# Optimization experiments

Measured on AMD Instinct MI355X. Metric: run time of the kernel, lower is better.

The kernel has to match this reference:

```python
import jax, jax.numpy as jnp
import numpy as np

N_NODES = 50000
IN_C, HID_C, OUT_C = 128, 128, 64
N_EDGES = 800000
N_LABEL = 200000
BN_EPS = 1e-5


def setup_inputs() -> dict:
    key = jax.random.key(0)
    ks = jax.random.split(key, 12)
    s = lambda fan_in: 1.0 / np.sqrt(fan_in)
    return {
        "x": jax.random.normal(ks[0], (N_NODES, IN_C), dtype=jnp.float32),
        "edge_index": jax.random.randint(ks[1], (2, N_EDGES), 0, N_NODES, dtype=jnp.int64),
        "edge_label_index": jax.random.randint(ks[2], (2, N_LABEL), 0, N_NODES, dtype=jnp.int64),
        # SAGEConv1: lin_l (neighbor branch, with bias) and lin_r (root branch, no bias)
        "W1l": jax.random.uniform(ks[3], (IN_C, HID_C), jnp.float32, -s(IN_C), s(IN_C)),
        "W1r": jax.random.uniform(ks[4], (IN_C, HID_C), jnp.float32, -s(IN_C), s(IN_C)),
        "b1": jax.random.uniform(ks[5], (HID_C,), jnp.float32, -s(IN_C), s(IN_C)),
        # BatchNorm1d(hidden)
        "gamma": jnp.ones((HID_C,), jnp.float32),
        "beta": jnp.zeros((HID_C,), jnp.float32),
        # SAGEConv2
        "W2l": jax.random.uniform(ks[6], (HID_C, OUT_C), jnp.float32, -s(HID_C), s(HID_C)),
        "W2r": jax.random.uniform(ks[7], (HID_C, OUT_C), jnp.float32, -s(HID_C), s(HID_C)),
        "b2": jax.random.uniform(ks[8], (OUT_C,), jnp.float32, -s(HID_C), s(HID_C)),
    }


def _sage_conv(x, edge_index, Wl, Wr, b):
    # PyG SAGEConv(aggr='mean'): out = lin_l(mean_{j->i} x_j) + lin_r(x_i)
    src, dst = edge_index[0], edge_index[1]
    n = x.shape[0]
    agg = jax.ops.segment_sum(x[src], dst, num_segments=n)          # [N, C]
    cnt = jax.ops.segment_sum(jnp.ones((src.shape[0],), x.dtype), dst, num_segments=n)
    mean = agg / jnp.maximum(cnt, 1.0)[:, None]                     # isolated nodes -> 0
    return mean @ Wl + x @ Wr + b


def _batchnorm(h, gamma, beta):
    mu = jnp.mean(h, axis=0)
    var = jnp.mean((h - mu) ** 2, axis=0)  # biased variance (torch BN training math)
    return gamma * (h - mu) * jax.lax.rsqrt(var + BN_EPS) + beta


def reference(x, edge_index, edge_label_index, W1l, W1r, b1, gamma, beta, W2l, W2r, b2):
    h = _sage_conv(x, edge_index, W1l, W1r, b1)
    h = jax.nn.relu(_batchnorm(h, gamma, beta))
    # dropout is identity in inference mode
    z = _sage_conv(h, edge_index, W2l, W2r, b2)
    src = z[edge_label_index[0]]
    dst = z[edge_label_index[1]]
    return jnp.sum(src * dst, axis=-1)  # [E_label]
```

## Files before the change

kernel.cpp:

```cpp
#include <hip/hip_runtime.h>

constexpr int N_NODES = 50000;
constexpr int IN_C    = 128;
constexpr int HID_C   = 128;
constexpr int OUT_C   = 64;
constexpr int N_EDGES = 800000;
constexpr int N_LABEL = 200000;
constexpr float BN_EPS = 1e-5f;
constexpr int NCHUNK  = (N_NODES + 256) / 256 + 1;
constexpr int BN_BLOCKS = 512;
constexpr int BN_RPH    = 13;

typedef __attribute__((ext_vector_type(8))) short bf16x8;
typedef __attribute__((ext_vector_type(4))) float f32x4;

__device__ __forceinline__ float bf_lo(unsigned v) {
    union { unsigned u; float f; } t; t.u = v << 16; return t.f;
}
__device__ __forceinline__ float bf_hi(unsigned v) {
    union { unsigned u; float f; } t; t.u = v & 0xffff0000u; return t.f;
}
__device__ __forceinline__ unsigned short f2bf(float f) {
    union { float f; unsigned u; } t; t.f = f;
    unsigned r = t.u + 0x7fffu + ((t.u >> 16) & 1u);
    return (unsigned short)(r >> 16);
}
__device__ __forceinline__ unsigned pack2bf(float a, float b) {
    return (unsigned)f2bf(a) | ((unsigned)f2bf(b) << 16);
}

__device__ __forceinline__ float fp8_f32(unsigned b) {
    union { unsigned u; float f; } t;
    t.u = ((b & 0x80u) << 24) | ((b & 0x7Fu) << 20);
    return t.f * 0x1p120f;
}
__device__ __forceinline__ unsigned f32_fp8(float x) {
    union { float f; unsigned u; } t; t.f = x * 0x1p-120f;
    unsigned au = t.u & 0x7FFFFFFFu;
    unsigned r = au + 0x7FFFFu + ((au >> 20) & 1u);
    return ((r >> 20) & 0x7Fu) | ((t.u >> 24) & 0x80u);
}

__global__ void zero_kernel(int* __restrict__ ideg, float* __restrict__ sums) {
    int i = blockIdx.x * 256 + threadIdx.x;
    if (i < 50432) ideg[i] = 0;
    if (i < 256) sums[i] = 0.f;
}

__global__ void hist_kernel(const int* __restrict__ dst, int* __restrict__ deg,
                            int* __restrict__ rank) {
    int e = blockIdx.x * blockDim.x + threadIdx.x;
    if (e < N_EDGES) rank[e] = atomicAdd(&deg[dst[e]], 1);
}

__global__ void chunk_sum_kernel(const int* __restrict__ deg, int* __restrict__ bsum) {
    int i = blockIdx.x * 256 + threadIdx.x;
    int v = deg[i];
    #pragma unroll
    for (int o = 32; o > 0; o >>= 1) v += __shfl_down(v, o, 64);
    __shared__ int ws[4];
    if ((threadIdx.x & 63) == 0) ws[threadIdx.x >> 6] = v;
    __syncthreads();
    if (threadIdx.x == 0) bsum[blockIdx.x] = ws[0] + ws[1] + ws[2] + ws[3];
}

__global__ void scan_bsum_kernel(const int* __restrict__ bsum, int* __restrict__ boff) {
    __shared__ int t[256];
    int tid = threadIdx.x;
    t[tid] = (tid < NCHUNK) ? bsum[tid] : 0;
    __syncthreads();
    for (int o = 1; o < 256; o <<= 1) {
        int v = t[tid];
        int add = (tid >= o) ? t[tid - o] : 0;
        __syncthreads();
        t[tid] = v + add;
        __syncthreads();
    }
    boff[tid] = (tid == 0) ? 0 : t[tid - 1];
}

__global__ void scan_final_kernel(const int* __restrict__ deg, const int* __restrict__ boff,
                                  int* __restrict__ off) {
    __shared__ int t[256];
    int tid = threadIdx.x;
    int i = blockIdx.x * 256 + tid;
    int d = deg[i];
    t[tid] = d;
    __syncthreads();
    for (int o = 1; o < 256; o <<= 1) {
        int v = t[tid];
        int add = (tid >= o) ? t[tid - o] : 0;
        __syncthreads();
        t[tid] = v + add;
        __syncthreads();
    }
    int excl = boff[blockIdx.x] + t[tid] - d;
    if (i <= N_NODES) off[i] = excl;
}

__global__ void scatter_kernel(const int* __restrict__ src, const int* __restrict__ dst,
                               const int* __restrict__ off, const int* __restrict__ rank,
                               int* __restrict__ csr_src) {
    int e = blockIdx.x * blockDim.x + threadIdx.x;
    if (e < N_EDGES) csr_src[off[dst[e]] + rank[e]] = src[e];
}

__global__ void prep_B(const float* __restrict__ Wl, const float* __restrict__ Wr,
                       short* __restrict__ Bp, int C) {
    int f = blockIdx.x * 256 + threadIdx.x;
    if (f >= 128 * C) return;
    int HALF = C >> 1;
    int j = f & 7;
    int l = (f >> 3) & 63;
    int ktnt = f >> 9;
    int kt = ktnt & 3, nt = ktnt >> 2;
    int n = nt * 16 + (l & 15);
    int k = kt * 32 + ((l >> 4) << 3) + j;
    float v = (n < HALF) ? Wl[k * HALF + n] : Wr[k * HALF + (n - HALF)];
    Bp[f] = (short)f2bf(v);
}

template <int MODE>
__global__ __launch_bounds__(256) void mfma_gemm(
    const void* __restrict__ Ain, const short* __restrict__ Bp,
    const float* __restrict__ bias, const float* __restrict__ ss,
    unsigned char* __restrict__ outFp8,
    unsigned short* __restrict__ outL16,
    unsigned short* __restrict__ outH16)
{
    constexpr int C    = (MODE == 0) ? 256 : 128;
    constexpr int NT   = C / 16;
    constexpr int HALF = C / 2;
    constexpr int CHUNKS = 128 * C / 8;

    __shared__ short sB[128 * C];

    {
        const float4* bp4 = reinterpret_cast<const float4*>(Bp);
        float4* sb4 = reinterpret_cast<float4*>(sB);
        #pragma unroll
        for (int i = 0; i < CHUNKS / 256; ++i)
            sb4[i * 256 + threadIdx.x] = bp4[i * 256 + threadIdx.x];
    }

    int tid  = threadIdx.x;
    int wid  = tid >> 6, lane = tid & 63;
    int m0   = blockIdx.x * 64 + wid * 16;
    int row  = m0 + (lane & 15);
    int rowc = (row < N_NODES) ? row : (N_NODES - 1);
    int kbase = (lane >> 4) * 8;

    bf16x8 a[4];
    #pragma unroll
    for (int kt = 0; kt < 4; ++kt) {
        int k0 = kt * 32 + kbase;
        float v[8];
        if (MODE == 0) {
            const float* ap = (const float*)Ain + (long long)rowc * 128;
            float4 u0 = *reinterpret_cast<const float4*>(ap + k0);
            float4 u1 = *reinterpret_cast<const float4*>(ap + k0 + 4);
            v[0]=u0.x; v[1]=u0.y; v[2]=u0.z; v[3]=u0.w;
            v[4]=u1.x; v[5]=u1.y; v[6]=u1.z; v[7]=u1.w;
        } else {
            const unsigned short* ap = (const unsigned short*)Ain + (long long)rowc * 128;
            uint4 w = *reinterpret_cast<const uint4*>(ap + k0);
            v[0]=bf_lo(w.x); v[1]=bf_hi(w.x); v[2]=bf_lo(w.y); v[3]=bf_hi(w.y);
            v[4]=bf_lo(w.z); v[5]=bf_hi(w.z); v[6]=bf_lo(w.w); v[7]=bf_hi(w.w);
            float4 s0 = *reinterpret_cast<const float4*>(ss + k0);
            float4 s1 = *reinterpret_cast<const float4*>(ss + k0 + 4);
            float4 t0 = *reinterpret_cast<const float4*>(ss + 128 + k0);
            float4 t1 = *reinterpret_cast<const float4*>(ss + 128 + k0 + 4);
            float sc[8] = {s0.x, s0.y, s0.z, s0.w, s1.x, s1.y, s1.z, s1.w};
            float sh[8] = {t0.x, t0.y, t0.z, t0.w, t1.x, t1.y, t1.z, t1.w};
            #pragma unroll
            for (int j = 0; j < 8; ++j) v[j] = fmaxf(v[j] * sc[j] + sh[j], 0.f);
        }
        #pragma unroll
        for (int j = 0; j < 8; ++j) a[kt][j] = (short)f2bf(v[j]);
    }

    __syncthreads();

    f32x4 acc[NT] = {};
    #pragma unroll
    for (int kt = 0; kt < 4; ++kt) {
        #pragma unroll
        for (int nt = 0; nt < NT; ++nt) {
            bf16x8 b = *reinterpret_cast<const bf16x8*>(
                sB + ((((nt << 2) + kt) * 64 + lane) << 3));
            acc[nt] = __builtin_amdgcn_mfma_f32_16x16x32_bf16(a[kt], b, acc[nt], 0, 0, 0);
        }
    }

    int r0 = m0 + ((lane >> 4) << 2);
    int nl = lane & 15;
    #pragma unroll
    for (int nt = 0; nt < NT; ++nt) {
        int col = nt * 16 + nl;
        float bb = (col >= HALF) ? bias[col - HALF] : 0.f;
        #pragma unroll
        for (int j = 0; j < 4; ++j) {
            int r = r0 + j;
            if (r >= N_NODES) continue;
            float vv = acc[nt][j];
            if (MODE == 0) {
                if (col < HALF) outFp8[(long long)r * 128 + col] = (unsigned char)f32_fp8(vv);
                else            outH16[(long long)r * 128 + (col - HALF)] = f2bf(vv + bb);
            } else {
                if (col < HALF) outL16[(long long)r * 64 + col] = f2bf(vv);
                else            outH16[(long long)r * 64 + (col - HALF)] = f2bf(vv + bb);
            }
        }
    }
}

__global__ __launch_bounds__(256) void agg_mean_add_128(
    const int* __restrict__ off, const int* __restrict__ csr_src,
    const uint2* __restrict__ y8, uint4* __restrict__ h4) {
    int node = blockIdx.x * 4 + (threadIdx.x >> 6);
    if (node >= N_NODES) return;
    int lane = threadIdx.x & 63;
    int grp  = lane >> 4;
    int c8   = lane & 15;
    int beg = off[node], end = off[node + 1];
    float s[8] = {0.f, 0.f, 0.f, 0.f, 0.f, 0.f, 0.f, 0.f};
    int i = beg + grp;
    for (; i + 4 < end; i += 8) {
        uint2 v0 = y8[(long long)csr_src[i]     * 16 + c8];
        uint2 v1 = y8[(long long)csr_src[i + 4] * 16 + c8];
        #pragma unroll
        for (int j = 0; j < 4; ++j) {
            s[j]     += fp8_f32((v0.x >> (8 * j)) & 0xFFu) + fp8_f32((v1.x >> (8 * j)) & 0xFFu);
            s[4 + j] += fp8_f32((v0.y >> (8 * j)) & 0xFFu) + fp8_f32((v1.y >> (8 * j)) & 0xFFu);
        }
    }
    for (; i < end; i += 4) {
        uint2 v0 = y8[(long long)csr_src[i] * 16 + c8];
        #pragma unroll
        for (int j = 0; j < 4; ++j) {
            s[j]     += fp8_f32((v0.x >> (8 * j)) & 0xFFu);
            s[4 + j] += fp8_f32((v0.y >> (8 * j)) & 0xFFu);
        }
    }
    #pragma unroll
    for (int j = 0; j < 8; ++j) {
        s[j] += __shfl_down(s[j], 16);
        s[j] += __shfl_down(s[j], 32);
    }
    if (grp == 0) {
        float inv = (end > beg) ? 1.0f / (float)(end - beg) : 0.f;
        uint4 hv = h4[(long long)node * 16 + c8];
        hv.x = pack2bf(bf_lo(hv.x) + s[0] * inv, bf_hi(hv.x) + s[1] * inv);
        hv.y = pack2bf(bf_lo(hv.y) + s[2] * inv, bf_hi(hv.y) + s[3] * inv);
        hv.z = pack2bf(bf_lo(hv.z) + s[4] * inv, bf_hi(hv.z) + s[5] * inv);
        hv.w = pack2bf(bf_lo(hv.w) + s[6] * inv, bf_hi(hv.w) + s[7] * inv);
        h4[(long long)node * 16 + c8] = hv;
    }
}

__global__ __launch_bounds__(256) void bn_stats_partial(
    const uint2* __restrict__ h2, float* __restrict__ partial) {
    int tid = threadIdx.x;
    int wid = tid >> 6;
    int lane = tid & 63;
    int half = lane >> 5;
    int c4   = lane & 31;
    int hw   = (blockIdx.x << 3) + (wid << 1) + half;
    int r0   = hw * BN_RPH;

    uint2 v[BN_RPH];
    #pragma unroll
    for (int j = 0; j < BN_RPH; ++j) {
        int r = r0 + j;
        v[j] = (r < N_NODES) ? h2[(long long)r * 32 + c4] : uint2{0u, 0u};
    }
    float s[4] = {0.f, 0.f, 0.f, 0.f}, q[4] = {0.f, 0.f, 0.f, 0.f};
    #pragma unroll
    for (int j = 0; j < BN_RPH; ++j) {
        float a0 = bf_lo(v[j].x), a1 = bf_hi(v[j].x);
        float a2 = bf_lo(v[j].y), a3 = bf_hi(v[j].y);
        s[0] += a0; q[0] += a0 * a0;
        s[1] += a1; q[1] += a1 * a1;
        s[2] += a2; q[2] += a2 * a2;
        s[3] += a3; q[3] += a3 * a3;
    }
    #pragma unroll
    for (int j = 0; j < 4; ++j) {
        s[j] += __shfl_down(s[j], 32);
        q[j] += __shfl_down(q[j], 32);
    }
    __shared__ float ls[4][32][8];
    if (half == 0) {
        #pragma unroll
        for (int j = 0; j < 4; ++j) { ls[wid][c4][j] = s[j]; ls[wid][c4][4 + j] = q[j]; }
    }
    __syncthreads();
    if (tid < 32) {
        #pragma unroll
        for (int j = 0; j < 8; ++j) {
            float a = ls[0][tid][j] + ls[1][tid][j] + ls[2][tid][j] + ls[3][tid][j];
            partial[blockIdx.x * 256 + (j < 4 ? 0 : 128) + tid * 4 + (j & 3)] = a;
        }
    }
}

__global__ void bn_stats_reduce(const float* __restrict__ partial,
                                float* __restrict__ sums) {
    int t = threadIdx.x;
    int b0 = blockIdx.x * (BN_BLOCKS / 16);
    float a = 0.f;
    #pragma unroll 8
    for (int b = b0; b < b0 + BN_BLOCKS / 16; ++b)
        a += partial[b * 256 + t];
    atomicAdd(&sums[t], a);
}

__global__ void bn_finalize_kernel(const float* __restrict__ sums,
                                   const float* __restrict__ gamma,
                                   const float* __restrict__ beta,
                                   float* __restrict__ ss) {
    int c = threadIdx.x;
    float mu  = sums[c] * (1.0f / N_NODES);
    float var = sums[128 + c] * (1.0f / N_NODES) - mu * mu;
    float sc = gamma[c] * rsqrtf(var + BN_EPS);
    ss[c] = sc;
    ss[128 + c] = beta[c] - mu * sc;
}

__global__ __launch_bounds__(256) void agg_mean_add_64(
    const int* __restrict__ off, const int* __restrict__ csr_src,
    const uint2* __restrict__ t2l2, const uint2* __restrict__ t2r2,
    uint2* __restrict__ z2) {
    int node = blockIdx.x * 4 + (threadIdx.x >> 6);
    if (node >= N_NODES) return;
    int lane = threadIdx.x & 63;
    int grp  = lane >> 4;
    int c8   = lane & 15;
    int beg = off[node], end = off[node + 1];
    float s0 = 0.f, s1 = 0.f, s2 = 0.f, s3 = 0.f;
    int i = beg + grp;
    for (; i + 4 < end; i += 8) {
        uint2 v0 = t2l2[(long long)csr_src[i]     * 16 + c8];
        uint2 v1 = t2l2[(long long)csr_src[i + 4] * 16 + c8];
        s0 += bf_lo(v0.x) + bf_lo(v1.x);
        s1 += bf_hi(v0.x) + bf_hi(v1.x);
        s2 += bf_lo(v0.y) + bf_lo(v1.y);
        s3 += bf_hi(v0.y) + bf_hi(v1.y);
    }
    for (; i < end; i += 4) {
        uint2 v0 = t2l2[(long long)csr_src[i] * 16 + c8];
        s0 += bf_lo(v0.x); s1 += bf_hi(v0.x);
        s2 += bf_lo(v0.y); s3 += bf_hi(v0.y);
    }
    s0 += __shfl_down(s0, 16); s1 += __shfl_down(s1, 16);
    s2 += __shfl_down(s2, 16); s3 += __shfl_down(s3, 16);
    s0 += __shfl_down(s0, 32); s1 += __shfl_down(s1, 32);
    s2 += __shfl_down(s2, 32); s3 += __shfl_down(s3, 32);
    if (grp == 0) {
        float inv = (end > beg) ? 1.0f / (float)(end - beg) : 0.f;
        uint2 rv = t2r2[(long long)node * 16 + c8];
        uint2 o;
        o.x = pack2bf(bf_lo(rv.x) + s0 * inv, bf_hi(rv.x) + s1 * inv);
        o.y = pack2bf(bf_lo(rv.y) + s2 * inv, bf_hi(rv.y) + s3 * inv);
        z2[(long long)node * 16 + c8] = o;
    }
}

__global__ void edge_dot_kernel(const int* __restrict__ eli,
                                const unsigned short* __restrict__ z,
                                float* __restrict__ out) {
    long long gid = (long long)blockIdx.x * blockDim.x + threadIdx.x;
    int l = (int)(gid >> 4);
    int lane = (int)(gid & 15);
    if (l >= N_LABEL) return;
    int s = eli[l];
    int d = eli[N_LABEL + l];
    uint2 av = *reinterpret_cast<const uint2*>(z + (long long)s * 64 + lane * 4);
    uint2 bv = *reinterpret_cast<const uint2*>(z + (long long)d * 64 + lane * 4);
    float p = bf_lo(av.x) * bf_lo(bv.x) + bf_hi(av.x) * bf_hi(bv.x)
            + bf_lo(av.y) * bf_lo(bv.y) + bf_hi(av.y) * bf_hi(bv.y);
    p += __shfl_down(p, 8, 16);
    p += __shfl_down(p, 4, 16);
    p += __shfl_down(p, 2, 16);
    p += __shfl_down(p, 1, 16);
    if (lane == 0) out[l] = p;
}

extern "C" void kernel_launch(void* const* d_in, const int* in_sizes, int n_in,
                              void* d_out, int out_size, void* d_ws, size_t ws_size,
                              hipStream_t stream) {
    const float* x     = (const float*)d_in[0];
    const int*   ei    = (const int*)d_in[1];
    const int*   eli   = (const int*)d_in[2];
    const float* W1l   = (const float*)d_in[3];
    const float* W1r   = (const float*)d_in[4];
    const float* b1    = (const float*)d_in[5];
    const float* gamma = (const float*)d_in[6];
    const float* beta  = (const float*)d_in[7];
    const float* W2l   = (const float*)d_in[8];
    const float* W2r   = (const float*)d_in[9];
    const float* b2    = (const float*)d_in[10];
    float* out = (float*)d_out;

    const int* src  = ei;
    const int* dstv = ei + N_EDGES;

    int* ideg  = (int*)d_ws;
    int* ioff  = ideg + 50432;
    int* ibsum = ioff + 50056;
    int* iboff = ibsum + 256;
    int* icsr  = iboff + 256;
    unsigned char*  y1  = (unsigned char*)(icsr + 800000);
    unsigned short* h   = (unsigned short*)(y1 + 6400000);
    unsigned short* t2l = h + 6400000;
    unsigned short* t2r = t2l + 3200000;
    unsigned short* z   = t2r + 3200000;
    float* sums = (float*)(z + 3200000);
    float* ss   = sums + 256;
    short* Bp1  = (short*)(ss + 256);
    short* Bp2  = Bp1 + 32768;
    float* bnpart = (float*)(Bp2 + 16384);
    int* irank = (int*)y1;

    zero_kernel<<<(50432 + 255) / 256, 256, 0, stream>>>(ideg, sums);

    prep_B<<<(128 * 256 + 255) / 256, 256, 0, stream>>>(W1l, W1r, Bp1, 256);
    prep_B<<<(128 * 128 + 255) / 256, 256, 0, stream>>>(W2l, W2r, Bp2, 128);

    hist_kernel<<<(N_EDGES + 255) / 256, 256, 0, stream>>>(dstv, ideg, irank);
    chunk_sum_kernel<<<NCHUNK, 256, 0, stream>>>(ideg, ibsum);
    scan_bsum_kernel<<<1, 256, 0, stream>>>(ibsum, iboff);
    scan_final_kernel<<<NCHUNK, 256, 0, stream>>>(ideg, iboff, ioff);
    scatter_kernel<<<(N_EDGES + 255) / 256, 256, 0, stream>>>(src, dstv, ioff, irank, icsr);

    const int GEMM_GRID = (N_NODES + 63) / 64;

    mfma_gemm<0><<<GEMM_GRID, 256, 0, stream>>>(x, Bp1, b1, ss, y1, nullptr, h);
    agg_mean_add_128<<<(N_NODES + 3) / 4, 256, 0, stream>>>(
        ioff, icsr, (const uint2*)y1, (uint4*)h);

    bn_stats_partial<<<BN_BLOCKS, 256, 0, stream>>>((const uint2*)h, bnpart);
    bn_stats_reduce<<<16, 256, 0, stream>>>(bnpart, sums);
    bn_finalize_kernel<<<1, 128, 0, stream>>>(sums, gamma, beta, ss);

    mfma_gemm<1><<<GEMM_GRID, 256, 0, stream>>>(h, Bp2, b2, ss, nullptr, t2l, t2r);
    agg_mean_add_64<<<(N_NODES + 3) / 4, 256, 0, stream>>>(
        ioff, icsr, (const uint2*)t2l, (const uint2*)t2r, (uint2*)z);

    edge_dot_kernel<<<((long long)N_LABEL * 16 + 255) / 256, 256, 0, stream>>>(eli, z, out);
}
```

Measured before the change: 187.9 us.

## Fuse BatchNorm statistics into layer-1 aggregation and merge setup kernels

Accumulates per-channel sum and sum-of-squares inside the first mean-aggregation kernel, whose blocks now each process 32 nodes. This removes the separate bn_stats_partial pass that re-read the whole hidden matrix. The zeroing and both weight-packing kernels are merged into one launch, and the GEMM blocks grow to 512 threads covering 128 rows. In exchange, the partial-stats buffer grows to one slot per aggregation block, there are fewer aggregation blocks to spread across the GPU, and each block runs a serial loop over its nodes.

```diff
diff --git a/kernel.cpp b/kernel.cpp
--- a/kernel.cpp
+++ b/kernel.cpp
@@ -8,8 +8,7 @@
 constexpr int N_LABEL = 200000;
 constexpr float BN_EPS = 1e-5f;
 constexpr int NCHUNK  = (N_NODES + 256) / 256 + 1;
-constexpr int BN_BLOCKS = 512;
-constexpr int BN_RPH    = 13;
+constexpr int AGG_BLOCKS = (N_NODES + 31) / 32;
 
 typedef __attribute__((ext_vector_type(8))) short bf16x8;
 typedef __attribute__((ext_vector_type(4))) float f32x4;
@@ -41,10 +40,32 @@
     return ((r >> 20) & 0x7Fu) | ((t.u >> 24) & 0x80u);
 }
 
-__global__ void zero_kernel(int* __restrict__ ideg, float* __restrict__ sums) {
+__global__ void setup_kernel(int* __restrict__ ideg, float* __restrict__ sums,
+                             const float* __restrict__ W1l, const float* __restrict__ W1r,
+                             short* __restrict__ Bp1,
+                             const float* __restrict__ W2l, const float* __restrict__ W2r,
+                             short* __restrict__ Bp2) {
     int i = blockIdx.x * 256 + threadIdx.x;
     if (i < 50432) ideg[i] = 0;
     if (i < 256) sums[i] = 0.f;
+    int j = i & 7;
+    int l = (i >> 3) & 63;
+    int ktnt = i >> 9;
+    int kt = ktnt & 3;
+    int nl = l & 15, kk = ((l >> 4) << 3) + j;
+    int k = kt * 32 + kk;
+    if (i < 32768) {
+        int nt = ktnt >> 2;
+        int n = nt * 16 + nl;
+        float v = (n < 128) ? W1l[k * 128 + n] : W1r[k * 128 + (n - 128)];
+        Bp1[i] = (short)f2bf(v);
+    }
+    if (i < 16384) {
+        int nt = ktnt >> 2;
+        int n = nt * 16 + nl;
+        float v = (n < 64) ? W2l[k * 64 + n] : W2r[k * 64 + (n - 64)];
+        Bp2[i] = (short)f2bf(v);
+    }
 }
 
 __global__ void hist_kernel(const int* __restrict__ dst, int* __restrict__ deg,
@@ -105,23 +126,8 @@
     if (e < N_EDGES) csr_src[off[dst[e]] + rank[e]] = src[e];
 }
 
-__global__ void prep_B(const float* __restrict__ Wl, const float* __restrict__ Wr,
-                       short* __restrict__ Bp, int C) {
-    int f = blockIdx.x * 256 + threadIdx.x;
-    if (f >= 128 * C) return;
-    int HALF = C >> 1;
-    int j = f & 7;
-    int l = (f >> 3) & 63;
-    int ktnt = f >> 9;
-    int kt = ktnt & 3, nt = ktnt >> 2;
-    int n = nt * 16 + (l & 15);
-    int k = kt * 32 + ((l >> 4) << 3) + j;
-    float v = (n < HALF) ? Wl[k * HALF + n] : Wr[k * HALF + (n - HALF)];
-    Bp[f] = (short)f2bf(v);
-}
-
 template <int MODE>
-__global__ __launch_bounds__(256) void mfma_gemm(
+__global__ __launch_bounds__(512) void mfma_gemm(
     const void* __restrict__ Ain, const short* __restrict__ Bp,
     const float* __restrict__ bias, const float* __restrict__ ss,
     unsigned char* __restrict__ outFp8,
@@ -139,13 +145,13 @@
         const float4* bp4 = reinterpret_cast<const float4*>(Bp);
         float4* sb4 = reinterpret_cast<float4*>(sB);
         #pragma unroll
-        for (int i = 0; i < CHUNKS / 256; ++i)
-            sb4[i * 256 + threadIdx.x] = bp4[i * 256 + threadIdx.x];
+        for (int i = 0; i < CHUNKS / 512; ++i)
+            sb4[i * 512 + threadIdx.x] = bp4[i * 512 + threadIdx.x];
     }
 
     int tid  = threadIdx.x;
     int wid  = tid >> 6, lane = tid & 63;
-    int m0   = blockIdx.x * 64 + wid * 16;
+    int m0   = blockIdx.x * 128 + wid * 16;
     int row  = m0 + (lane & 15);
     int rowc = (row < N_NODES) ? row : (N_NODES - 1);
     int kbase = (lane >> 4) * 8;
@@ -214,103 +220,82 @@
     }
 }
 
-__global__ __launch_bounds__(256) void agg_mean_add_128(
+__global__ __launch_bounds__(256) void agg_mean_add_128_bn(
     const int* __restrict__ off, const int* __restrict__ csr_src,
-    const uint2* __restrict__ y8, uint4* __restrict__ h4) {
-    int node = blockIdx.x * 4 + (threadIdx.x >> 6);
-    if (node >= N_NODES) return;
-    int lane = threadIdx.x & 63;
+    const uint2* __restrict__ y8, uint4* __restrict__ h4,
+    float* __restrict__ partial) {
+    int tid  = threadIdx.x;
+    int wid  = tid >> 6;
+    int lane = tid & 63;
     int grp  = lane >> 4;
     int c8   = lane & 15;
-    int beg = off[node], end = off[node + 1];
-    float s[8] = {0.f, 0.f, 0.f, 0.f, 0.f, 0.f, 0.f, 0.f};
-    int i = beg + grp;
-    for (; i + 4 < end; i += 8) {
-        uint2 v0 = y8[(long long)csr_src[i]     * 16 + c8];
-        uint2 v1 = y8[(long long)csr_src[i + 4] * 16 + c8];
-        #pragma unroll
-        for (int j = 0; j < 4; ++j) {
-            s[j]     += fp8_f32((v0.x >> (8 * j)) & 0xFFu) + fp8_f32((v1.x >> (8 * j)) & 0xFFu);
-            s[4 + j] += fp8_f32((v0.y >> (8 * j)) & 0xFFu) + fp8_f32((v1.y >> (8 * j)) & 0xFFu);
-        }
-    }
-    for (; i < end; i += 4) {
-        uint2 v0 = y8[(long long)csr_src[i] * 16 + c8];
-        #pragma unroll
-        for (int j = 0; j < 4; ++j) {
-            s[j]     += fp8_f32((v0.x >> (8 * j)) & 0xFFu);
-            s[4 + j] += fp8_f32((v0.y >> (8 * j)) & 0xFFu);
-        }
-    }
-    #pragma unroll
-    for (int j = 0; j < 8; ++j) {
-        s[j] += __shfl_down(s[j], 16);
-        s[j] += __shfl_down(s[j], 32);
-    }
+    float rs[8] = {0.f,0.f,0.f,0.f,0.f,0.f,0.f,0.f};
+    float rq[8] = {0.f,0.f,0.f,0.f,0.f,0.f,0.f,0.f};
+
+    for (int it = 0; it < 8; ++it) {
+        int node = blockIdx.x * 32 + it * 4 + wid;
+        if (node >= N_NODES) break;
+        int beg = off[node], end = off[node + 1];
+        float s[8] = {0.f,0.f,0.f,0.f,0.f,0.f,0.f,0.f};
+        int i = beg + grp;
+        for (; i + 4 < end; i += 8) {
+            uint2 v0 = y8[(long long)csr_src[i]     * 16 + c8];
+            uint2 v1 = y8[(long long)csr_src[i + 4] * 16 + c8];
+            #pragma unroll
+            for (int j = 0; j < 4; ++j) {
+                s[j]     += fp8_f32((v0.x >> (8 * j)) & 0xFFu) + fp8_f32((v1.x >> (8 * j)) & 0xFFu);
+                s[4 + j] += fp8_f32((v0.y >> (8 * j)) & 0xFFu) + fp8_f32((v1.y >> (8 * j)) & 0xFFu);
+            }
+        }
+        for (; i < end; i += 4) {
+            uint2 v0 = y8[(long long)csr_src[i] * 16 + c8];
+            #pragma unroll
+            for (int j = 0; j < 4; ++j) {
+                s[j]     += fp8_f32((v0.x >> (8 * j)) & 0xFFu);
+                s[4 + j] += fp8_f32((v0.y >> (8 * j)) & 0xFFu);
+            }
+        }
+        #pragma unroll
+        for (int j = 0; j < 8; ++j) {
+            s[j] += __shfl_down(s[j], 16);
+            s[j] += __shfl_down(s[j], 32);
+        }
+        if (grp == 0) {
+            float inv = (end > beg) ? 1.0f / (float)(end - beg) : 0.f;
+            uint4 hv = h4[(long long)node * 16 + c8];
+            hv.x = pack2bf(bf_lo(hv.x) + s[0] * inv, bf_hi(hv.x) + s[1] * inv);
+            hv.y = pack2bf(bf_lo(hv.y) + s[2] * inv, bf_hi(hv.y) + s[3] * inv);
+            hv.z = pack2bf(bf_lo(hv.z) + s[4] * inv, bf_hi(hv.z) + s[5] * inv);
+            hv.w = pack2bf(bf_lo(hv.w) + s[6] * inv, bf_hi(hv.w) + s[7] * inv);
+            h4[(long long)node * 16 + c8] = hv;
+            float rr[8] = {bf_lo(hv.x), bf_hi(hv.x), bf_lo(hv.y), bf_hi(hv.y),
+                           bf_lo(hv.z), bf_hi(hv.z), bf_lo(hv.w), bf_hi(hv.w)};
+            #pragma unroll
+            for (int j = 0; j < 8; ++j) { rs[j] += rr[j]; rq[j] += rr[j] * rr[j]; }
+        }
+    }
+
+    __shared__ float ls[4][256];
     if (grp == 0) {
-        float inv = (end > beg) ? 1.0f / (float)(end - beg) : 0.f;
-        uint4 hv = h4[(long long)node * 16 + c8];
-        hv.x = pack2bf(bf_lo(hv.x) + s[0] * inv, bf_hi(hv.x) + s[1] * inv);
-        hv.y = pack2bf(bf_lo(hv.y) + s[2] * inv, bf_hi(hv.y) + s[3] * inv);
-        hv.z = pack2bf(bf_lo(hv.z) + s[4] * inv, bf_hi(hv.z) + s[5] * inv);
-        hv.w = pack2bf(bf_lo(hv.w) + s[6] * inv, bf_hi(hv.w) + s[7] * inv);
-        h4[(long long)node * 16 + c8] = hv;
-    }
-}
-
-__global__ __launch_bounds__(256) void bn_stats_partial(
-    const uint2* __restrict__ h2, float* __restrict__ partial) {
-    int tid = threadIdx.x;
-    int wid = tid >> 6;
-    int lane = tid & 63;
-    int half = lane >> 5;
-    int c4   = lane & 31;
-    int hw   = (blockIdx.x << 3) + (wid << 1) + half;
-    int r0   = hw * BN_RPH;
-
-    uint2 v[BN_RPH];
-    #pragma unroll
-    for (int j = 0; j < BN_RPH; ++j) {
-        int r = r0 + j;
-        v[j] = (r < N_NODES) ? h2[(long long)r * 32 + c4] : uint2{0u, 0u};
-    }
-    float s[4] = {0.f, 0.f, 0.f, 0.f}, q[4] = {0.f, 0.f, 0.f, 0.f};
-    #pragma unroll
-    for (int j = 0; j < BN_RPH; ++j) {
-        float a0 = bf_lo(v[j].x), a1 = bf_hi(v[j].x);
-        float a2 = bf_lo(v[j].y), a3 = bf_hi(v[j].y);
-        s[0] += a0; q[0] += a0 * a0;
-        s[1] += a1; q[1] += a1 * a1;
-        s[2] += a2; q[2] += a2 * a2;
-        s[3] += a3; q[3] += a3 * a3;
-    }
-    #pragma unroll
-    for (int j = 0; j < 4; ++j) {
-        s[j] += __shfl_down(s[j], 32);
-        q[j] += __shfl_down(q[j], 32);
-    }
-    __shared__ float ls[4][32][8];
-    if (half == 0) {
-        #pragma unroll
-        for (int j = 0; j < 4; ++j) { ls[wid][c4][j] = s[j]; ls[wid][c4][4 + j] = q[j]; }
+        #pragma unroll
+        for (int j = 0; j < 8; ++j) {
+            ls[wid][c8 * 8 + j]       = rs[j];
+            ls[wid][128 + c8 * 8 + j] = rq[j];
+        }
     }
     __syncthreads();
-    if (tid < 32) {
-        #pragma unroll
-        for (int j = 0; j < 8; ++j) {
-            float a = ls[0][tid][j] + ls[1][tid][j] + ls[2][tid][j] + ls[3][tid][j];
-            partial[blockIdx.x * 256 + (j < 4 ? 0 : 128) + tid * 4 + (j & 3)] = a;
-        }
-    }
+    partial[blockIdx.x * 256 + tid] =
+        ls[0][tid] + ls[1][tid] + ls[2][tid] + ls[3][tid];
 }
 
 __global__ void bn_stats_reduce(const float* __restrict__ partial,
                                 float* __restrict__ sums) {
     int t = threadIdx.x;
-    int b0 = blockIdx.x * (BN_BLOCKS / 16);
+    int per = (AGG_BLOCKS + 15) / 16;
+    int b0 = blockIdx.x * per;
+    int b1 = min(b0 + per, AGG_BLOCKS);
     float a = 0.f;
-    #pragma unroll 8
-    for (int b = b0; b < b0 + BN_BLOCKS / 16; ++b)
+    for (int b = b0; b < b1; ++b)
         a += partial[b * 256 + t];
     atomicAdd(&sums[t], a);
 }
@@ -422,10 +407,8 @@
     float* bnpart = (float*)(Bp2 + 16384);
     int* irank = (int*)y1;
 
-    zero_kernel<<<(50432 + 255) / 256, 256, 0, stream>>>(ideg, sums);
-
-    prep_B<<<(128 * 256 + 255) / 256, 256, 0, stream>>>(W1l, W1r, Bp1, 256);
-    prep_B<<<(128 * 128 + 255) / 256, 256, 0, stream>>>(W2l, W2r, Bp2, 128);
+    setup_kernel<<<(50432 + 255) / 256, 256, 0, stream>>>(
+        ideg, sums, W1l, W1r, Bp1, W2l, W2r, Bp2);
 
     hist_kernel<<<(N_EDGES + 255) / 256, 256, 0, stream>>>(dstv, ideg, irank);
     chunk_sum_kernel<<<NCHUNK, 256, 0, stream>>>(ideg, ibsum);
@@ -433,17 +416,16 @@
     scan_final_kernel<<<NCHUNK, 256, 0, stream>>>(ideg, iboff, ioff);
     scatter_kernel<<<(N_EDGES + 255) / 256, 256, 0, stream>>>(src, dstv, ioff, irank, icsr);
 
-    const int GEMM_GRID = (N_NODES + 63) / 64;
-
-    mfma_gemm<0><<<GEMM_GRID, 256, 0, stream>>>(x, Bp1, b1, ss, y1, nullptr, h);
-    agg_mean_add_128<<<(N_NODES + 3) / 4, 256, 0, stream>>>(
-        ioff, icsr, (const uint2*)y1, (uint4*)h);
-
-    bn_stats_partial<<<BN_BLOCKS, 256, 0, stream>>>((const uint2*)h, bnpart);
+    const int GEMM_GRID = (N_NODES + 127) / 128;
+
+    mfma_gemm<0><<<GEMM_GRID, 512, 0, stream>>>(x, Bp1, b1, ss, y1, nullptr, h);
+    agg_mean_add_128_bn<<<AGG_BLOCKS, 256, 0, stream>>>(
+        ioff, icsr, (const uint2*)y1, (uint4*)h, bnpart);
+
     bn_stats_reduce<<<16, 256, 0, stream>>>(bnpart, sums);
     bn_finalize_kernel<<<1, 128, 0, stream>>>(sums, gamma, beta, ss);
 
-    mfma_gemm<1><<<GEMM_GRID, 256, 0, stream>>>(h, Bp2, b2, ss, nullptr, t2l, t2r);
+    mfma_gemm<1><<<GEMM_GRID, 512, 0, stream>>>(h, Bp2, b2, ss, nullptr, t2l, t2r);
     agg_mean_add_64<<<(N_NODES + 3) / 4, 256, 0, stream>>>(
         ioff, icsr, (const uint2*)t2l, (const uint2*)t2r, (uint2*)z);
 
```

After: 208.1 us. +10.7%, slower.
